# Kernel optimization log

Hardware: AMD Instinct MI355X
Metric: run time of the kernel (lower is better)

The kernel has to match this reference:

```python
import jax, jax.numpy as jnp
import numpy as np
import math

N = 100000      # nodes
E = 1600000     # edges
D = 128         # in_channels
C = 256         # number of dominant-set cliques
HID = 64        # mlp_hidden
RATIO = 0.8
K = int(math.ceil(RATIO * N))  # 80000 topk nodes per view


def setup_inputs() -> dict:
    key = jax.random.key(0)
    ks = jax.random.split(key, 18)
    s = 0.05
    return {
        "x": jax.random.normal(ks[0], (N, D), jnp.float32),
        "edge_index": jax.random.randint(ks[1], (2, E), 0, N, dtype=jnp.int32),
        "batch": jnp.zeros((N,), jnp.int32),
        "cluster_id": jax.random.randint(ks[2], (N,), 0, C, dtype=jnp.int32),
        # MLP scorer: Linear(D,HID) -> ReLU -> Linear(HID,1)
        "mlp_w1": jax.random.normal(ks[3], (D, HID), jnp.float32) * s,
        "mlp_b1": jnp.zeros((HID,), jnp.float32),
        "mlp_w2": jax.random.normal(ks[4], (HID, 1), jnp.float32) * s,
        "mlp_b2": jnp.zeros((1,), jnp.float32),
        # GATConv(D, 1, heads=1)
        "gat_w": jax.random.normal(ks[5], (D, 1), jnp.float32) * s,
        "gat_a_src": jax.random.normal(ks[6], (1,), jnp.float32) * s,
        "gat_a_dst": jax.random.normal(ks[7], (1,), jnp.float32) * s,
        "gat_b": jnp.zeros((1,), jnp.float32),
        # InterChannelGCN attention Linear(2D,1) split into fine/coarse halves
        "att_w_fine": jax.random.normal(ks[8], (D,), jnp.float32) * s,
        "att_w_coarse": jax.random.normal(ks[9], (D,), jnp.float32) * s,
        "att_b": jnp.zeros((1,), jnp.float32),
        # InterChannelGCN transform Linear(D,D)
        "trans_w": jax.random.normal(ks[10], (D, D), jnp.float32) * s,
        "trans_b": jnp.zeros((D,), jnp.float32),
    }


def _inter_channel_gcn(h_fine, H_coarse, R, wa, wb, ab, tw, tb):
    # attention(Linear(2D,1)) on concat(h_fine_i, H_coarse_j) == h_fine@wa + H_coarse@wb + b
    scores = h_fine @ wa[:, None] + (H_coarse @ wb)[None, :] + ab[0]   # [K, C]
    attn = jax.nn.softmax(scores * R, axis=-1)                          # mask-by-multiply, as original
    out = attn @ H_coarse + h_fine                                      # add_self=True
    return jax.nn.relu(out @ tw + tb)                                   # normalize=False


def reference(x, edge_index, batch, cluster_id,
              mlp_w1, mlp_b1, mlp_w2, mlp_b2,
              gat_w, gat_a_src, gat_a_dst, gat_b,
              att_w_fine, att_w_coarse, att_b, trans_w, trans_b):
    src, dst = edge_index[0], edge_index[1]

    # --- DominantClustering('avg'): cluster means as coarse features ---
    counts = jax.ops.segment_sum(jnp.ones((N,), jnp.float32), cluster_id, num_segments=C)
    Hcoarse = jax.ops.segment_sum(x, cluster_id, num_segments=C) / jnp.maximum(counts, 1.0)[:, None]

    # --- feature view: MLP score + topk ---
    feature_score = (jax.nn.relu(x @ mlp_w1 + mlp_b1) @ mlp_w2 + mlp_b2)[:, 0]   # [N]
    _, feat_idx = jax.lax.top_k(feature_score, K)
    feature_view3 = x[feat_idx]
    R_feat = jax.nn.one_hot(cluster_id[feat_idx], C, dtype=x.dtype)              # relationship matrix
    fuse1 = _inter_channel_gcn(feature_view3, Hcoarse, R_feat,
                               att_w_fine, att_w_coarse, att_b, trans_w, trans_b)

    # --- local view: GATConv(D,1,heads=1) score + topk ---
    h = x @ gat_w                                                                 # [N,1]
    e = jax.nn.leaky_relu(gat_a_src[0] * h[src, 0] + gat_a_dst[0] * h[dst, 0], 0.2)  # [E]
    m = jax.ops.segment_max(e, dst, num_segments=N)
    ex = jnp.exp(e - m[dst])
    den = jax.ops.segment_sum(ex, dst, num_segments=N)
    alpha = ex / jnp.maximum(den[dst], 1e-16)
    localview_score = jax.ops.segment_sum(alpha * h[src, 0], dst, num_segments=N) + gat_b[0]
    _, local_idx = jax.lax.top_k(localview_score, K)
    local_view1 = x[local_idx]
    R_local = jax.nn.one_hot(cluster_id[local_idx], C, dtype=x.dtype)
    fuse2 = _inter_channel_gcn(local_view1, Hcoarse, R_local,
                               att_w_fine, att_w_coarse, att_b, trans_w, trans_b)

    # --- union, edge filtering + remapping (padded fixed shapes) ---
    in_feat = jnp.zeros((N,), bool).at[feat_idx].set(True)
    in_local = jnp.zeros((N,), bool).at[local_idx].set(True)
    union = in_feat | in_local
    mapping = jnp.where(union, jnp.cumsum(union.astype(jnp.int32)) - 1, -1)
    m0, m1 = mapping[src], mapping[dst]
    valid = (m0 >= 0) & (m1 >= 0)
    edge_index_topk = jnp.where(valid[None, :], jnp.stack([m0, m1]), -1)          # [2,E], -1 = dropped

    # --- fused features (faithful to original's fuse1/fuse2 index swap) ---
    A = jnp.zeros((N, D), x.dtype).at[feat_idx].set(fuse2)    # fuse2 indexed by feature topk position
    B = jnp.zeros((N, D), x.dtype).at[local_idx].set(fuse1)   # fuse1 indexed by local topk position
    both = in_feat & in_local
    Fp = jnp.where(both[:, None], (A + B) * 0.5, A + B)
    Fp = jnp.where(union[:, None], Fp, 0.0)                   # [N,D], zero outside union

    new_batch = jnp.where(union, batch, -1)
    return Fp, edge_index_topk, new_batch
```

## Files before the change

### kernel.cpp

```cpp
#include <hip/hip_runtime.h>
#include <hip/hip_bf16.h>
#include <stdint.h>

#define N 100000
#define E_ 1600000
#define D 128
#define C_ 256
#define HID 64
#define KSEL 80000
#define NB 4096
#define CHUNK 1024
#define NCHUNK ((N + CHUNK - 1) / CHUNK)
#define CSEG 32
#define NBK 782
#define BCAP 2560
#define RMAX 2048

typedef __attribute__((ext_vector_type(8))) short bf16x8;
typedef __attribute__((ext_vector_type(4))) float f32x4;

__device__ __forceinline__ unsigned enc_f(float f) {
  unsigned b = __float_as_uint(f);
  return (b & 0x80000000u) ? ~b : (b | 0x80000000u);
}
__device__ __forceinline__ float dec_f(unsigned u) {
  unsigned b = (u & 0x80000000u) ? (u ^ 0x80000000u) : ~u;
  return __uint_as_float(b);
}

__device__ __forceinline__ unsigned short f2bf(float f) {
  unsigned u = __float_as_uint(f);
  unsigned r = u + 0x7FFFu + ((u >> 16) & 1u);
  return (unsigned short)(r >> 16);
}

__global__ __launch_bounds__(256) void k_hist_cluster(const int* __restrict__ cid, int* __restrict__ ccount) {
  int n = blockIdx.x * 256 + threadIdx.x;
  if (n < N) atomicAdd(&ccount[cid[n]], 1);
}

__global__ __launch_bounds__(1024) void k_scan_small(const int* __restrict__ in0, int* __restrict__ out0, int n) {
  __shared__ int sums[1024];
  const int* in = in0 + (size_t)blockIdx.x * n;
  int* out = out0 + (size_t)blockIdx.x * n;
  int t = threadIdx.x;
  int per = (n + 1023) / 1024;
  int base = t * per;
  int loc = 0;
  for (int k = 0; k < per; ++k) { int i = base + k; if (i < n) loc += in[i]; }
  sums[t] = loc; __syncthreads();
  for (int off = 1; off < 1024; off <<= 1) {
    int v = (t >= off) ? sums[t - off] : 0;
    __syncthreads();
    sums[t] += v;
    __syncthreads();
  }
  int run = (t == 0) ? 0 : sums[t - 1];
  for (int k = 0; k < per; ++k) { int i = base + k; if (i < n) { out[i] = run; run += in[i]; } }
}

__global__ __launch_bounds__(256) void k_scatter_cluster(const int* __restrict__ cid, const int* __restrict__ cstart,
                                                         int* __restrict__ ccur, int* __restrict__ cslot) {
  int n = blockIdx.x * 256 + threadIdx.x;
  if (n < N) {
    int c = cid[n];
    int p = cstart[c] + atomicAdd(&ccur[c], 1);
    cslot[p] = n;
  }
}

__global__ __launch_bounds__(128) void k_cluster_partial(const float* __restrict__ x, const int* __restrict__ cstart,
                                                         const int* __restrict__ ccount, const int* __restrict__ cslot,
                                                         float* __restrict__ Hc) {
  int c = blockIdx.x >> 5;
  int s = blockIdx.x & (CSEG - 1);
  int d = threadIdx.x;
  int st = cstart[c], cnt = ccount[c];
  int seg = (cnt + CSEG - 1) / CSEG;
  int lo = s * seg;
  int hi = min(cnt, lo + seg);
  if (lo >= hi) return;
  float acc = 0.f;
  int k = lo;
  for (; k + 2 <= hi; k += 2) {
    int n0 = cslot[st + k], n1 = cslot[st + k + 1];
    float v0 = x[(size_t)n0 * D + d];
    float v1 = x[(size_t)n1 * D + d];
    acc += v0 + v1;
  }
  if (k < hi) acc += x[(size_t)cslot[st + k] * D + d];
  atomicAdd(&Hc[(size_t)c * D + d], acc);
}

__global__ __launch_bounds__(128) void k_mean_gdot(const int* __restrict__ ccount, const float* __restrict__ wb,
                                                   float* __restrict__ Hc, float* __restrict__ gdot) {
  __shared__ float red[128];
  int c = blockIdx.x, d = threadIdx.x;
  float hv = Hc[(size_t)c * D + d] / (float)max(ccount[c], 1);
  Hc[(size_t)c * D + d] = hv;
  red[d] = hv * wb[d];
  __syncthreads();
  if (d < 64) {
    float v = red[d] + red[d + 64];
    for (int off = 32; off; off >>= 1) v += __shfl_down(v, off);
    if (d == 0) gdot[c] = v;
  }
}

__global__ __launch_bounds__(128) void k_S_SW_HW(const float* __restrict__ Hc, const float* __restrict__ tw,
                                                 float* __restrict__ SW, float* __restrict__ HW) {
  __shared__ float Sl[128];
  int b = blockIdx.x, t = threadIdx.x;
  if (b == 0) {
    float s = 0.f;
    for (int c = 0; c < C_; ++c) s += Hc[(size_t)c * D + t];
    Sl[t] = s;
    __syncthreads();
    float acc = 0.f;
    for (int d = 0; d < D; ++d) acc = fmaf(Sl[d], tw[(size_t)d * D + t], acc);
    SW[t] = acc;
  } else {
    const float* src = Hc + (size_t)(b - 1) * D;
    float acc = 0.f;
    for (int d = 0; d < D; ++d) acc = fmaf(src[d], tw[(size_t)d * D + t], acc);
    HW[(size_t)(b - 1) * D + t] = acc;
  }
}

__global__ __launch_bounds__(128) void k_twT(const float* __restrict__ tw, unsigned short* __restrict__ twT) {
  int k = blockIdx.x;
  int o = threadIdx.x;
  twT[(size_t)o * D + k] = f2bf(tw[(size_t)k * D + o]);
}

__global__ __launch_bounds__(256, 4) void k_score64(const float* __restrict__ x, const float* __restrict__ w1,
                                                    const float* __restrict__ b1, const float* __restrict__ w2,
                                                    const float* __restrict__ b2, const float* __restrict__ gw,
                                                    const float* __restrict__ wa, float* __restrict__ scoreF,
                                                    float* __restrict__ hg, float* __restrict__ aDot) {
  __shared__ float xld[64 * D];
  int tid = threadIdx.x;
  int base = blockIdx.x * 64;
#pragma unroll
  for (int k = 0; k < 8; ++k) {
    int i = k * 256 + tid;
    int r = i >> 5, cc = i & 31;
    int n = base + r;
    float4 v = make_float4(0.f, 0.f, 0.f, 0.f);
    if (n < N) v = ((const float4*)(x + (size_t)n * D))[cc];
    ((float4*)xld)[r * 32 + (cc ^ (r & 7))] = v;
  }
  __syncthreads();

  int rg = tid >> 4;
  int cg = tid & 15;
  int r0 = rg * 4;
  int c4 = cg * 4;
  float acc[4][4] = {};
  float4 wc0 = *(const float4*)(w1 + (size_t)0 * HID + c4);
  float4 wc1 = *(const float4*)(w1 + (size_t)1 * HID + c4);
  float4 wc2 = *(const float4*)(w1 + (size_t)2 * HID + c4);
  float4 wc3 = *(const float4*)(w1 + (size_t)3 * HID + c4);
  for (int d4 = 0; d4 < D; d4 += 4) {
    float4 wn0, wn1, wn2, wn3;
    if (d4 + 4 < D) {
      wn0 = *(const float4*)(w1 + (size_t)(d4 + 4) * HID + c4);
      wn1 = *(const float4*)(w1 + (size_t)(d4 + 5) * HID + c4);
      wn2 = *(const float4*)(w1 + (size_t)(d4 + 6) * HID + c4);
      wn3 = *(const float4*)(w1 + (size_t)(d4 + 7) * HID + c4);
    } else {
      wn0 = wn1 = wn2 = wn3 = make_float4(0.f, 0.f, 0.f, 0.f);
    }
    int j = d4 >> 2;
#pragma unroll
    for (int rr = 0; rr < 4; ++rr) {
      int row = r0 + rr;
      float4 xv = ((const float4*)xld)[row * 32 + (j ^ (row & 7))];
      acc[rr][0] = fmaf(xv.x, wc0.x, acc[rr][0]);
      acc[rr][1] = fmaf(xv.x, wc0.y, acc[rr][1]);
      acc[rr][2] = fmaf(xv.x, wc0.z, acc[rr][2]);
      acc[rr][3] = fmaf(xv.x, wc0.w, acc[rr][3]);
      acc[rr][0] = fmaf(xv.y, wc1.x, acc[rr][0]);
      acc[rr][1] = fmaf(xv.y, wc1.y, acc[rr][1]);
      acc[rr][2] = fmaf(xv.y, wc1.z, acc[rr][2]);
      acc[rr][3] = fmaf(xv.y, wc1.w, acc[rr][3]);
      acc[rr][0] = fmaf(xv.z, wc2.x, acc[rr][0]);
      acc[rr][1] = fmaf(xv.z, wc2.y, acc[rr][1]);
      acc[rr][2] = fmaf(xv.z, wc2.z, acc[rr][2]);
      acc[rr][3] = fmaf(xv.z, wc2.w, acc[rr][3]);
      acc[rr][0] = fmaf(xv.w, wc3.x, acc[rr][0]);
      acc[rr][1] = fmaf(xv.w, wc3.y, acc[rr][1]);
      acc[rr][2] = fmaf(xv.w, wc3.z, acc[rr][2]);
      acc[rr][3] = fmaf(xv.w, wc3.w, acc[rr][3]);
    }
    wc0 = wn0; wc1 = wn1; wc2 = wn2; wc3 = wn3;
  }

  float4 b1v = *(const float4*)(b1 + c4);
  float4 w2v = *(const float4*)(w2 + c4);
  float bb = b2[0];
#pragma unroll
  for (int rr = 0; rr < 4; ++rr) {
    float p = fmaxf(acc[rr][0] + b1v.x, 0.f) * w2v.x
            + fmaxf(acc[rr][1] + b1v.y, 0.f) * w2v.y
            + fmaxf(acc[rr][2] + b1v.z, 0.f) * w2v.z
            + fmaxf(acc[rr][3] + b1v.w, 0.f) * w2v.w;
#pragma unroll
    for (int off = 8; off; off >>= 1) p += __shfl_xor(p, off);
    if (cg == 0) {
      int n = base + r0 + rr;
      if (n < N) scoreF[n] = p + bb;
    }
  }

  float4 gwa = *(const float4*)(gw + c4);
  float4 gwb = *(const float4*)(gw + 64 + c4);
  float4 waa = *(const float4*)(wa + c4);
  float4 wab = *(const float4*)(wa + 64 + c4);
#pragma unroll
  for (int rr = 0; rr < 4; ++rr) {
    int row = r0 + rr;
    float4 xa = ((const float4*)xld)[row * 32 + (cg ^ (row & 7))];
    float4 xb = ((const float4*)xld)[row * 32 + ((cg + 16) ^ (row & 7))];
    float hp = xa.x * gwa.x + xa.y * gwa.y + xa.z * gwa.z + xa.w * gwa.w
             + xb.x * gwb.x + xb.y * gwb.y + xb.z * gwb.z + xb.w * gwb.w;
    float ap = xa.x * waa.x + xa.y * waa.y + xa.z * waa.z + xa.w * waa.w
             + xb.x * wab.x + xb.y * wab.y + xb.z * wab.z + xb.w * wab.w;
#pragma unroll
    for (int off = 8; off; off >>= 1) {
      hp += __shfl_xor(hp, off);
      ap += __shfl_xor(ap, off);
    }
    if (cg == 0) {
      int n = base + row;
      if (n < N) { hg[n] = hp; aDot[n] = ap; }
    }
  }
}

__global__ __launch_bounds__(1024) void k_escatter(const int* __restrict__ ei, const float* __restrict__ hg,
                                                   const float* __restrict__ asrc, const float* __restrict__ adst,
                                                   int* __restrict__ gcnt, uint2* __restrict__ payload) {
  __shared__ int lcnt[NBK];
  __shared__ int lbase[NBK];
  int tid = threadIdx.x;
  for (int i = tid; i < NBK; i += 1024) lcnt[i] = 0;
  int e0 = blockIdx.x * 8192;
  int es[8], ed[8];
#pragma unroll
  for (int k = 0; k < 8; ++k) {
    int e = e0 + k * 1024 + tid;
    bool v = (e < E_);
    es[k] = v ? ei[e] : -1;
    ed[k] = v ? ei[E_ + e] : -1;
  }
  __syncthreads();
#pragma unroll
  for (int k = 0; k < 8; ++k)
    if (ed[k] >= 0) atomicAdd(&lcnt[ed[k] >> 7], 1);
  __syncthreads();
  for (int i = tid; i < NBK; i += 1024) {
    int c = lcnt[i];
    lbase[i] = c ? atomicAdd(&gcnt[i], c) : 0;
    lcnt[i] = 0;
  }
  __syncthreads();
  float as = asrc[0], ad = adst[0];
#pragma unroll
  for (int k = 0; k < 8; ++k) {
    if (ed[k] < 0) continue;
    int s = es[k], d = ed[k];
    int b = d >> 7, dl = d & 127;
    float z = as * hg[s] + ad * hg[d];
    float ev = (z > 0.f) ? z : 0.2f * z;
    int pos = lbase[b] + atomicAdd(&lcnt[b], 1);
    if (pos < BCAP) {
      uint2 rec;
      rec.x = __float_as_uint(ev);
      rec.y = (unsigned)s | ((unsigned)dl << 24);
      payload[(size_t)b * BCAP + pos] = rec;
    }
  }
}

__global__ __launch_bounds__(256) void k_esoftmax(const uint2* __restrict__ payload, const int* __restrict__ gcnt,
                                                  const float* __restrict__ hg, const float* __restrict__ gb,
                                                  float* __restrict__ scoreL) {
  __shared__ unsigned mS[128];
  __shared__ float dS[128];
  __shared__ float nS[128];
  int b = blockIdx.x;
  int tid = threadIdx.x;
  if (tid < 128) { mS[tid] = 0u; dS[tid] = 0.f; nS[tid] = 0.f; }
  __syncthreads();
  int cnt = min(gcnt[b], BCAP);
  const uint2* bp = payload + (size_t)b * BCAP;
  for (int i = tid; i < cnt; i += 256) {
    uint2 r = bp[i];
    atomicMax(&mS[r.y >> 24], enc_f(__uint_as_float(r.x)));
  }
  __syncthreads();
  for (int i = tid; i < cnt; i += 256) {
    uint2 r = bp[i];
    int d = r.y >> 24;
    float ex = expf(__uint_as_float(r.x) - dec_f(mS[d]));
    atomicAdd(&dS[d], ex);
  }
  __syncthreads();
  for (int i = tid; i < cnt; i += 256) {
    uint2 r = bp[i];
    int d = r.y >> 24;
    float ex = expf(__uint_as_float(r.x) - dec_f(mS[d]));
    float alpha = ex / fmaxf(dS[d], 1e-16f);
    float h = hg[r.y & 0xFFFFFFu];
    atomicAdd(&nS[d], alpha * h);
  }
  __syncthreads();
  if (tid < 128) {
    int dst = b * 128 + tid;
    if (dst < N) scoreL[dst] = nS[tid] + gb[0];
  }
}

__global__ __launch_bounds__(256) void k_minmax2(const float* __restrict__ sc2, unsigned* __restrict__ mm) {
  __shared__ unsigned smx[256], smn[256];
  int v = blockIdx.y;
  const float* sc = sc2 + (size_t)v * N;
  int t = threadIdx.x; int n = blockIdx.x * 256 + t;
  unsigned val = (n < N) ? enc_f(sc[n]) : 0u;
  smx[t] = (n < N) ? val : 0u;
  smn[t] = (n < N) ? val : 0xFFFFFFFFu;
  __syncthreads();
  for (int off = 128; off; off >>= 1) {
    if (t < off) {
      smx[t] = max(smx[t], smx[t + off]);
      smn[t] = min(smn[t], smn[t + off]);
    }
    __syncthreads();
  }
  if (t == 0) { atomicMax(&mm[v], smx[0]); atomicMin(&mm[2 + v], smn[0]); }
}

__global__ __launch_bounds__(256) void k_bucket_hist2(const float* __restrict__ sc2, const unsigned* __restrict__ mm,
                                                      int* __restrict__ bucket2, int* __restrict__ hist2) {
  int v = blockIdx.y;
  int n = blockIdx.x * 256 + threadIdx.x;
  if (n >= N) return;
  const float* sc = sc2 + (size_t)v * N;
  float smax = dec_f(mm[v]), smin = dec_f(mm[2 + v]);
  float range = smax - smin;
  float scale = (range > 0.f) ? ((float)NB / range) : 0.f;
  float t = (smax - sc[n]) * scale;
  int b = (int)t;
  b = b < 0 ? 0 : (b > NB - 1 ? NB - 1 : b);
  bucket2[(size_t)v * N + n] = b;
  atomicAdd(&hist2[v * NB + b], 1);
}

__global__ __launch_bounds__(256) void k_bucket_scatter2(const int* __restrict__ bucket2, const int* __restrict__ start2,
                                                         int* __restrict__ cur2, int* __restrict__ slot2) {
  int v = blockIdx.y;
  int n = blockIdx.x * 256 + threadIdx.x;
  if (n >= N) return;
  int b = bucket2[(size_t)v * N + n];
  slot2[(size_t)v * N + start2[v * NB + b] + atomicAdd(&cur2[v * NB + b], 1)] = n;
}

__global__ __launch_bounds__(64) void k_bucket_rank3(const float* __restrict__ sc2, const int* __restrict__ start2,
                                                     const int* __restrict__ hist2, const int* __restrict__ slot2,
                                                     int* __restrict__ rank2, int* __restrict__ sorted2) {
  __shared__ unsigned long long keys[RMAX];
  int v = blockIdx.y;
  int b = blockIdx.x;
  int st = start2[v * NB + b], cnt = hist2[v * NB + b];
  if (cnt == 0) return;
  const float* sc = sc2 + (size_t)v * N;
  const int* slot = slot2 + (size_t)v * N;
  int* rank = rank2 + (size_t)v * N;
  int* sorted = sorted2 + (size_t)v * N;
  int tid = threadIdx.x;
  if (cnt <= RMAX) {
    for (int i = tid; i < cnt; i += 64) {
      int m = slot[st + i];
      keys[i] = (((unsigned long long)(~enc_f(sc[m]))) << 32) | (unsigned)m;
    }
    __syncthreads();
    for (int i = tid; i < cnt; i += 64) {
      unsigned long long mykey = keys[i];
      int r = 0;
      for (int j = 0; j < cnt; ++j) r += (keys[j] < mykey) ? 1 : 0;
      int m = (int)(mykey & 0xFFFFFFFFu);
      rank[m] = st + r;
      sorted[st + r] = m;
    }
  } else {
    for (int i = tid; i < cnt; i += 64) {
      int m = slot[st + i];
      unsigned long long mykey = (((unsigned long long)(~enc_f(sc[m]))) << 32) | (unsigned)m;
      int r = 0;
      for (int j = 0; j < cnt; ++j) {
        int mj = slot[st + j];
        unsigned long long k = (((unsigned long long)(~enc_f(sc[mj]))) << 32) | (unsigned)mj;
        r += (k < mykey) ? 1 : 0;
      }
      rank[m] = st + r;
      sorted[st + r] = m;
    }
  }
}

__global__ __launch_bounds__(1024) void k_union_chunksum(const int* __restrict__ rankF, const int* __restrict__ rankL,
                                                         int* __restrict__ csum) {
  __shared__ int red[1024];
  int t = threadIdx.x; int i = blockIdx.x * 1024 + t;
  int u = (i < N) ? (((rankF[i] < KSEL) || (rankL[i] < KSEL)) ? 1 : 0) : 0;
  red[t] = u; __syncthreads();
  for (int off = 512; off; off >>= 1) { if (t < off) red[t] += red[t + off]; __syncthreads(); }
  if (t == 0) csum[blockIdx.x] = red[0];
}

__global__ __launch_bounds__(1024) void k_union_map(const int* __restrict__ rankF, const int* __restrict__ rankL,
                                                    const int* __restrict__ cstart, const int* __restrict__ batch,
                                                    int* __restrict__ mapping, float* __restrict__ outBatch) {
  __shared__ int sums[1024];
  int t = threadIdx.x; int i = blockIdx.x * 1024 + t;
  int u = (i < N) ? (((rankF[i] < KSEL) || (rankL[i] < KSEL)) ? 1 : 0) : 0;
  sums[t] = u; __syncthreads();
  for (int off = 1; off < 1024; off <<= 1) {
    int v = (t >= off) ? sums[t - off] : 0;
    __syncthreads();
    sums[t] += v;
    __syncthreads();
  }
  if (i < N) {
    mapping[i] = u ? (cstart[blockIdx.x] + sums[t] - 1) : -1;
    outBatch[i] = u ? (float)batch[i] : -1.0f;
  }
}

__global__ __launch_bounds__(256) void k_edge_out(const int* __restrict__ ei, const int* __restrict__ mapping,
                                                  float* __restrict__ outE) {
  int e = blockIdx.x * 256 + threadIdx.x;
  if (e >= E_) return;
  int m0 = mapping[ei[e]], m1 = mapping[ei[E_ + e]];
  bool valid = (m0 >= 0) && (m1 >= 0);
  outE[e] = valid ? (float)m0 : -1.f;
  outE[E_ + e] = valid ? (float)m1 : -1.f;
}

__global__ __launch_bounds__(256) void k_zero_rows(const int* __restrict__ mapping, float* __restrict__ Fp) {
  int i = blockIdx.x * 256 + threadIdx.x;
  int n = i >> 5;
  if (n < N && mapping[n] < 0) ((float4*)Fp)[i] = make_float4(0.f, 0.f, 0.f, 0.f);
}

__global__ __launch_bounds__(256, 4) void k_fuse64(const float* __restrict__ x, const unsigned short* __restrict__ twT,
                                                   const float* __restrict__ tb, const float* __restrict__ SW,
                                                   const float* __restrict__ HW, const float* __restrict__ gdot,
                                                   const float* __restrict__ aDot, const int* __restrict__ cid,
                                                   const int* __restrict__ srcL, const int* __restrict__ tgtL,
                                                   const float* __restrict__ attb, const int* __restrict__ rankF,
                                                   float* __restrict__ Fp, int accum) {
  __shared__ __align__(16) unsigned xw[64 * 64];
  __shared__ float pq[64 * 2];
  __shared__ int mt[64 * 2];
  __shared__ int ft[64];
  int tid = threadIdx.x;
  int base = blockIdx.x * 64;
  if (tid < 64) {
    int ws = srcL[base + tid];
    int cc = cid[ws];
    int tg = tgtL[base + tid];
    mt[tid * 2] = cc;
    mt[tid * 2 + 1] = tg;
    ft[tid] = (rankF[tg] < KSEL) ? 1 : 0;
    float s = aDot[ws] + gdot[cc] + attb[0];
    float mx = fmaxf(s, 0.f);
    float esm = expf(s - mx), eom = expf(-mx);
    float dn = esm + 255.f * eom;
    pq[tid * 2] = esm / dn;
    pq[tid * 2 + 1] = eom / dn;
  }
#pragma unroll
  for (int k = 0; k < 8; ++k) {
    int i = k * 256 + tid;
    int r = i >> 5, c4 = i & 31;
    int ws = srcL[base + r];
    float4 v = ((const float4*)(x + (size_t)ws * D))[c4];
    uint2 pk;
    pk.x = (unsigned)f2bf(v.x) | ((unsigned)f2bf(v.y) << 16);
    pk.y = (unsigned)f2bf(v.z) | ((unsigned)f2bf(v.w) << 16);
    int u2 = r * 32 + (c4 ^ ((r & 7) << 1));
    ((uint2*)xw)[u2] = pk;
  }
  __syncthreads();

  int w = tid >> 6;
  int l = tid & 63;
  int nl = l & 15;
  int khalf = l >> 4;
  int row = w * 16 + nl;

  f32x4 acc[8] = {};
  const char* xbase = (const char*)xw + row * 256;
  unsigned rsw = (unsigned)((row & 7) << 4);
#pragma unroll
  for (int ks = 0; ks < 4; ++ks) {
    bf16x8 bfrag = *(const bf16x8*)(xbase + (((unsigned)(ks * 64 + khalf * 16)) ^ rsw));
#pragma unroll
    for (int ot = 0; ot < 8; ++ot) {
      bf16x8 afrag = *(const bf16x8*)(twT + (size_t)(ot * 16 + nl) * D + ks * 32 + khalf * 8);
      acc[ot] = __builtin_amdgcn_mfma_f32_16x16x32_bf16(afrag, bfrag, acc[ot], 0, 0, 0);
    }
  }

  float p = pq[row * 2], q = pq[row * 2 + 1];
  int cc = mt[row * 2];
  int tgt = mt[row * 2 + 1];
  int doAcc = accum && ft[row];
#pragma unroll
  for (int ot = 0; ot < 8; ++ot) {
    int ch = ot * 16 + khalf * 4;
    float4 tbv = *(const float4*)(tb + ch);
    float4 swv = *(const float4*)(SW + ch);
    float4 hw = *(const float4*)(HW + (size_t)cc * D + ch);
    float4 o;
    o.x = fmaxf(acc[ot][0] + tbv.x + q * swv.x + (p - q) * hw.x, 0.f);
    o.y = fmaxf(acc[ot][1] + tbv.y + q * swv.y + (p - q) * hw.y, 0.f);
    o.z = fmaxf(acc[ot][2] + tbv.z + q * swv.z + (p - q) * hw.z, 0.f);
    o.w = fmaxf(acc[ot][3] + tbv.w + q * swv.w + (p - q) * hw.w, 0.f);
    float4* dst = (float4*)(Fp + (size_t)tgt * D + ch);
    if (doAcc) {
      float4 old = *dst;
      o.x = (o.x + old.x) * 0.5f;
      o.y = (o.y + old.y) * 0.5f;
      o.z = (o.z + old.z) * 0.5f;
      o.w = (o.w + old.w) * 0.5f;
    }
    *dst = o;
  }
}

extern "C" void kernel_launch(void* const* d_in, const int* in_sizes, int n_in,
                              void* d_out, int out_size, void* d_ws, size_t ws_size,
                              hipStream_t stream) {
  const float* x   = (const float*)d_in[0];
  const int* ei    = (const int*)d_in[1];
  const int* batch = (const int*)d_in[2];
  const int* cid   = (const int*)d_in[3];
  const float* w1  = (const float*)d_in[4];
  const float* b1  = (const float*)d_in[5];
  const float* w2  = (const float*)d_in[6];
  const float* b2  = (const float*)d_in[7];
  const float* gw  = (const float*)d_in[8];
  const float* gas = (const float*)d_in[9];
  const float* gad = (const float*)d_in[10];
  const float* gb  = (const float*)d_in[11];
  const float* wa  = (const float*)d_in[12];
  const float* wb  = (const float*)d_in[13];
  const float* ab  = (const float*)d_in[14];
  const float* tw  = (const float*)d_in[15];
  const float* tb  = (const float*)d_in[16];
  (void)in_sizes; (void)n_in; (void)ws_size; (void)out_size;

  char* p = (char*)d_ws;
  auto alloc = [&](size_t bytes) -> char* {
    char* r = p;
    p += (bytes + 255) & ~(size_t)255;
    return r;
  };
  int* ccount    = (int*)alloc(C_ * 4);
  int* ccur      = (int*)alloc(C_ * 4);
  unsigned* mm   = (unsigned*)alloc(16);
  int* hist2     = (int*)alloc(2 * NB * 4);
  int* cur2      = (int*)alloc(2 * NB * 4);
  float* Hc      = (float*)alloc((size_t)C_ * D * 4);
  int* gcnt      = (int*)alloc(NBK * 4);
  size_t zeroBytes = (size_t)(p - (char*)d_ws);
  int* cstart   = (int*)alloc(C_ * 4);
  int* cslot    = (int*)alloc((size_t)N * 4);
  float* gdot   = (float*)alloc(C_ * 4);
  float* SW     = (float*)alloc(D * 4);
  float* HW     = (float*)alloc((size_t)C_ * D * 4);
  unsigned short* twT = (unsigned short*)alloc((size_t)D * D * 2);
  float* score2 = (float*)alloc((size_t)2 * N * 4);
  float* hg     = (float*)alloc((size_t)N * 4);
  float* aDot   = (float*)alloc((size_t)N * 4);
  uint2* payload = (uint2*)alloc((size_t)NBK * BCAP * 8);
  int* bucket2  = (int*)alloc((size_t)2 * N * 4);
  int* start2   = (int*)alloc(2 * NB * 4);
  int* slot2    = (int*)alloc((size_t)2 * N * 4);
  int* sorted2  = (int*)alloc((size_t)2 * N * 4);
  int* rank2    = (int*)alloc((size_t)2 * N * 4);
  int* csums    = (int*)alloc(NCHUNK * 4);
  int* cstarts  = (int*)alloc(NCHUNK * 4);
  int* mapping  = (int*)alloc((size_t)N * 4);

  float* scoreF = score2;
  float* scoreL = score2 + N;
  int* sortedF  = sorted2;
  int* sortedL  = sorted2 + N;
  int* rankF    = rank2;
  int* rankL    = rank2 + N;

  float* outF = (float*)d_out;
  float* outE = outF + (size_t)N * D;
  float* outB = outE + (size_t)2 * E_;

  hipMemsetAsync(d_ws, 0, zeroBytes, stream);
  hipMemsetAsync(mm + 2, 0xFF, 8, stream);

  k_hist_cluster<<<(N + 255) / 256, 256, 0, stream>>>(cid, ccount);
  k_scan_small<<<1, 1024, 0, stream>>>(ccount, cstart, C_);
  k_scatter_cluster<<<(N + 255) / 256, 256, 0, stream>>>(cid, cstart, ccur, cslot);
  k_cluster_partial<<<C_ * CSEG, 128, 0, stream>>>(x, cstart, ccount, cslot, Hc);
  k_mean_gdot<<<C_, 128, 0, stream>>>(ccount, wb, Hc, gdot);
  k_S_SW_HW<<<C_ + 1, 128, 0, stream>>>(Hc, tw, SW, HW);
  k_twT<<<D, D, 0, stream>>>(tw, twT);

  k_score64<<<(N + 63) / 64, 256, 0, stream>>>(x, w1, b1, w2, b2, gw, wa, scoreF, hg, aDot);
  k_escatter<<<(E_ + 8191) / 8192, 1024, 0, stream>>>(ei, hg, gas, gad, gcnt, payload);
  k_esoftmax<<<NBK, 256, 0, stream>>>(payload, gcnt, hg, gb, scoreL);

  dim3 g2((N + 255) / 256, 2);
  k_minmax2<<<g2, 256, 0, stream>>>(score2, mm);
  k_bucket_hist2<<<g2, 256, 0, stream>>>(score2, mm, bucket2, hist2);
  k_scan_small<<<2, 1024, 0, stream>>>(hist2, start2, NB);
  k_bucket_scatter2<<<g2, 256, 0, stream>>>(bucket2, start2, cur2, slot2);
  dim3 gr(NB, 2);
  k_bucket_rank3<<<gr, 64, 0, stream>>>(score2, start2, hist2, slot2, rank2, sorted2);

  k_union_chunksum<<<NCHUNK, 1024, 0, stream>>>(rankF, rankL, csums);
  k_scan_small<<<1, 1024, 0, stream>>>(csums, cstarts, NCHUNK);
  k_union_map<<<NCHUNK, 1024, 0, stream>>>(rankF, rankL, cstarts, batch, mapping, outB);
  k_edge_out<<<(E_ + 255) / 256, 256, 0, stream>>>(ei, mapping, outE);
  k_zero_rows<<<(N * 32 + 255) / 256, 256, 0, stream>>>(mapping, outF);

  k_fuse64<<<KSEL / 64, 256, 0, stream>>>(x, twT, tb, SW, HW, gdot, aDot, cid, sortedL, sortedF, ab, rankF, outF, 0);
  k_fuse64<<<KSEL / 64, 256, 0, stream>>>(x, twT, tb, SW, HW, gdot, aDot, cid, sortedF, sortedL, ab, rankF, outF, 1);
}
```

Baseline: 560.1 us.

## Fuse score min/max into producers and merge softmax passes

Computes the per-view score min/max inside the scoring and edge-softmax kernels using wave shuffles and shared atomics, which removes the separate minmax kernel launch and its re-read of the scores. The edge softmax now accumulates the numerator and denominator in one pass and divides at the end, so the third pass over the payload goes away. It also prefetches x rows from LDS into registers in the MLP loop and hoists the bf16 B fragments ahead of the MFMA loop in the fuse kernel. The trade-offs are higher register pressure and a final normalization step that differs slightly in rounding from the original per-edge alpha.

```diff
diff --git a/kernel.cpp b/kernel.cpp
--- a/kernel.cpp
+++ b/kernel.cpp
@@ -137,10 +137,13 @@
                                                     const float* __restrict__ b1, const float* __restrict__ w2,
                                                     const float* __restrict__ b2, const float* __restrict__ gw,
                                                     const float* __restrict__ wa, float* __restrict__ scoreF,
-                                                    float* __restrict__ hg, float* __restrict__ aDot) {
+                                                    float* __restrict__ hg, float* __restrict__ aDot,
+                                                    unsigned* __restrict__ mm) {
   __shared__ float xld[64 * D];
+  __shared__ unsigned bmm[2];
   int tid = threadIdx.x;
   int base = blockIdx.x * 64;
+  if (tid == 0) { bmm[0] = 0u; bmm[1] = 0xFFFFFFFFu; }
 #pragma unroll
   for (int k = 0; k < 8; ++k) {
     int i = k * 256 + tid;
@@ -161,21 +164,33 @@
   float4 wc1 = *(const float4*)(w1 + (size_t)1 * HID + c4);
   float4 wc2 = *(const float4*)(w1 + (size_t)2 * HID + c4);
   float4 wc3 = *(const float4*)(w1 + (size_t)3 * HID + c4);
+  float4 xc[4];
+#pragma unroll
+  for (int rr = 0; rr < 4; ++rr) {
+    int row = r0 + rr;
+    xc[rr] = ((const float4*)xld)[row * 32 + (row & 7)];
+  }
   for (int d4 = 0; d4 < D; d4 += 4) {
-    float4 wn0, wn1, wn2, wn3;
+    float4 wn0, wn1, wn2, wn3, xn[4];
     if (d4 + 4 < D) {
       wn0 = *(const float4*)(w1 + (size_t)(d4 + 4) * HID + c4);
       wn1 = *(const float4*)(w1 + (size_t)(d4 + 5) * HID + c4);
       wn2 = *(const float4*)(w1 + (size_t)(d4 + 6) * HID + c4);
       wn3 = *(const float4*)(w1 + (size_t)(d4 + 7) * HID + c4);
+      int jn = (d4 >> 2) + 1;
+#pragma unroll
+      for (int rr = 0; rr < 4; ++rr) {
+        int row = r0 + rr;
+        xn[rr] = ((const float4*)xld)[row * 32 + (jn ^ (row & 7))];
+      }
     } else {
       wn0 = wn1 = wn2 = wn3 = make_float4(0.f, 0.f, 0.f, 0.f);
-    }
-    int j = d4 >> 2;
+#pragma unroll
+      for (int rr = 0; rr < 4; ++rr) xn[rr] = make_float4(0.f, 0.f, 0.f, 0.f);
+    }
 #pragma unroll
     for (int rr = 0; rr < 4; ++rr) {
-      int row = r0 + rr;
-      float4 xv = ((const float4*)xld)[row * 32 + (j ^ (row & 7))];
+      float4 xv = xc[rr];
       acc[rr][0] = fmaf(xv.x, wc0.x, acc[rr][0]);
       acc[rr][1] = fmaf(xv.x, wc0.y, acc[rr][1]);
       acc[rr][2] = fmaf(xv.x, wc0.z, acc[rr][2]);
@@ -194,11 +209,14 @@
       acc[rr][3] = fmaf(xv.w, wc3.w, acc[rr][3]);
     }
     wc0 = wn0; wc1 = wn1; wc2 = wn2; wc3 = wn3;
+#pragma unroll
+    for (int rr = 0; rr < 4; ++rr) xc[rr] = xn[rr];
   }
 
   float4 b1v = *(const float4*)(b1 + c4);
   float4 w2v = *(const float4*)(w2 + c4);
   float bb = b2[0];
+  unsigned vmx = 0u, vmn = 0xFFFFFFFFu;
 #pragma unroll
   for (int rr = 0; rr < 4; ++rr) {
     float p = fmaxf(acc[rr][0] + b1v.x, 0.f) * w2v.x
@@ -209,9 +227,21 @@
     for (int off = 8; off; off >>= 1) p += __shfl_xor(p, off);
     if (cg == 0) {
       int n = base + r0 + rr;
-      if (n < N) scoreF[n] = p + bb;
-    }
-  }
+      if (n < N) {
+        float sf = p + bb;
+        scoreF[n] = sf;
+        unsigned e = enc_f(sf);
+        vmx = max(vmx, e);
+        vmn = min(vmn, e);
+      }
+    }
+  }
+#pragma unroll
+  for (int off = 32; off; off >>= 1) {
+    vmx = max(vmx, (unsigned)__shfl_xor((int)vmx, off));
+    vmn = min(vmn, (unsigned)__shfl_xor((int)vmn, off));
+  }
+  if ((tid & 63) == 0) { atomicMax(&bmm[0], vmx); atomicMin(&bmm[1], vmn); }
 
   float4 gwa = *(const float4*)(gw + c4);
   float4 gwb = *(const float4*)(gw + 64 + c4);
@@ -236,6 +266,8 @@
       if (n < N) { hg[n] = hp; aDot[n] = ap; }
     }
   }
+  __syncthreads();
+  if (tid == 0) { atomicMax(&mm[0], bmm[0]); atomicMin(&mm[2], bmm[1]); }
 }
 
 __global__ __launch_bounds__(1024) void k_escatter(const int* __restrict__ ei, const float* __restrict__ hg,
@@ -285,13 +317,15 @@
 
 __global__ __launch_bounds__(256) void k_esoftmax(const uint2* __restrict__ payload, const int* __restrict__ gcnt,
                                                   const float* __restrict__ hg, const float* __restrict__ gb,
-                                                  float* __restrict__ scoreL) {
+                                                  float* __restrict__ scoreL, unsigned* __restrict__ mm) {
   __shared__ unsigned mS[128];
   __shared__ float dS[128];
   __shared__ float nS[128];
+  __shared__ unsigned bmm[2];
   int b = blockIdx.x;
   int tid = threadIdx.x;
   if (tid < 128) { mS[tid] = 0u; dS[tid] = 0.f; nS[tid] = 0.f; }
+  if (tid == 0) { bmm[0] = 0u; bmm[1] = 0xFFFFFFFFu; }
   __syncthreads();
   int cnt = min(gcnt[b], BCAP);
   const uint2* bp = payload + (size_t)b * BCAP;
@@ -304,41 +338,29 @@
     uint2 r = bp[i];
     int d = r.y >> 24;
     float ex = expf(__uint_as_float(r.x) - dec_f(mS[d]));
+    float h = hg[r.y & 0xFFFFFFu];
     atomicAdd(&dS[d], ex);
-  }
-  __syncthreads();
-  for (int i = tid; i < cnt; i += 256) {
-    uint2 r = bp[i];
-    int d = r.y >> 24;
-    float ex = expf(__uint_as_float(r.x) - dec_f(mS[d]));
-    float alpha = ex / fmaxf(dS[d], 1e-16f);
-    float h = hg[r.y & 0xFFFFFFu];
-    atomicAdd(&nS[d], alpha * h);
-  }
-  __syncthreads();
+    atomicAdd(&nS[d], ex * h);
+  }
+  __syncthreads();
+  unsigned vmx = 0u, vmn = 0xFFFFFFFFu;
   if (tid < 128) {
     int dst = b * 128 + tid;
-    if (dst < N) scoreL[dst] = nS[tid] + gb[0];
-  }
-}
-
-__global__ __launch_bounds__(256) void k_minmax2(const float* __restrict__ sc2, unsigned* __restrict__ mm) {
-  __shared__ unsigned smx[256], smn[256];
-  int v = blockIdx.y;
-  const float* sc = sc2 + (size_t)v * N;
-  int t = threadIdx.x; int n = blockIdx.x * 256 + t;
-  unsigned val = (n < N) ? enc_f(sc[n]) : 0u;
-  smx[t] = (n < N) ? val : 0u;
-  smn[t] = (n < N) ? val : 0xFFFFFFFFu;
-  __syncthreads();
-  for (int off = 128; off; off >>= 1) {
-    if (t < off) {
-      smx[t] = max(smx[t], smx[t + off]);
-      smn[t] = min(smn[t], smn[t + off]);
-    }
-    __syncthreads();
-  }
-  if (t == 0) { atomicMax(&mm[v], smx[0]); atomicMin(&mm[2 + v], smn[0]); }
+    if (dst < N) {
+      float sl = nS[tid] / fmaxf(dS[tid], 1e-16f) + gb[0];
+      scoreL[dst] = sl;
+      unsigned e = enc_f(sl);
+      vmx = e; vmn = e;
+    }
+  }
+#pragma unroll
+  for (int off = 32; off; off >>= 1) {
+    vmx = max(vmx, (unsigned)__shfl_xor((int)vmx, off));
+    vmn = min(vmn, (unsigned)__shfl_xor((int)vmn, off));
+  }
+  if ((tid & 63) == 0) { atomicMax(&bmm[0], vmx); atomicMin(&bmm[1], vmn); }
+  __syncthreads();
+  if (tid == 0) { atomicMax(&mm[1], bmm[0]); atomicMin(&mm[3], bmm[1]); }
 }
 
 __global__ __launch_bounds__(256) void k_bucket_hist2(const float* __restrict__ sc2, const unsigned* __restrict__ mm,
@@ -504,13 +526,16 @@
   f32x4 acc[8] = {};
   const char* xbase = (const char*)xw + row * 256;
   unsigned rsw = (unsigned)((row & 7) << 4);
+  bf16x8 bfr[4];
+#pragma unroll
+  for (int ks = 0; ks < 4; ++ks)
+    bfr[ks] = *(const bf16x8*)(xbase + (((unsigned)(ks * 64 + khalf * 16)) ^ rsw));
 #pragma unroll
   for (int ks = 0; ks < 4; ++ks) {
-    bf16x8 bfrag = *(const bf16x8*)(xbase + (((unsigned)(ks * 64 + khalf * 16)) ^ rsw));
 #pragma unroll
     for (int ot = 0; ot < 8; ++ot) {
       bf16x8 afrag = *(const bf16x8*)(twT + (size_t)(ot * 16 + nl) * D + ks * 32 + khalf * 8);
-      acc[ot] = __builtin_amdgcn_mfma_f32_16x16x32_bf16(afrag, bfrag, acc[ot], 0, 0, 0);
+      acc[ot] = __builtin_amdgcn_mfma_f32_16x16x32_bf16(afrag, bfr[ks], acc[ot], 0, 0, 0);
     }
   }
 
@@ -618,12 +643,11 @@
   k_S_SW_HW<<<C_ + 1, 128, 0, stream>>>(Hc, tw, SW, HW);
   k_twT<<<D, D, 0, stream>>>(tw, twT);
 
-  k_score64<<<(N + 63) / 64, 256, 0, stream>>>(x, w1, b1, w2, b2, gw, wa, scoreF, hg, aDot);
+  k_score64<<<(N + 63) / 64, 256, 0, stream>>>(x, w1, b1, w2, b2, gw, wa, scoreF, hg, aDot, mm);
   k_escatter<<<(E_ + 8191) / 8192, 1024, 0, stream>>>(ei, hg, gas, gad, gcnt, payload);
-  k_esoftmax<<<NBK, 256, 0, stream>>>(payload, gcnt, hg, gb, scoreL);
+  k_esoftmax<<<NBK, 256, 0, stream>>>(payload, gcnt, hg, gb, scoreL, mm);
 
   dim3 g2((N + 255) / 256, 2);
-  k_minmax2<<<g2, 256, 0, stream>>>(score2, mm);
   k_bucket_hist2<<<g2, 256, 0, stream>>>(score2, mm, bucket2, hist2);
   k_scan_small<<<2, 1024, 0, stream>>>(hist2, start2, NB);
   k_bucket_scatter2<<<g2, 256, 0, stream>>>(bucket2, start2, cur2, slot2);
```

Result: no change. 566.4 us (+1.1%).
